# Kernel tuning notes

Measured on AMD Instinct MI355X. Metric: run time of the kernel, lower is better.

Reference implementation:

```python
import jax, jax.numpy as jnp
import numpy as np

B, S, D, E, K = 4, 2048, 1024, 8, 2


def setup_inputs() -> dict:
    key = jax.random.key(0)
    k1, k2, k3 = jax.random.split(key, 3)
    scale = 1.0 / np.sqrt(D)
    x = jax.random.normal(k1, (B, S, D), dtype=jnp.float32)
    Wg = jax.random.normal(k2, (D, E), dtype=jnp.float32) * scale
    bg = jnp.zeros((E,), dtype=jnp.float32)
    We = jax.random.normal(k3, (E, D, D), dtype=jnp.float32) * scale
    be = jnp.zeros((E, D), dtype=jnp.float32)
    return {"x": x, "Wg": Wg, "bg": bg, "We": We, "be": be}


def reference(x, Wg, bg, We, be):
    # gate scores: [B, S, E]
    gate_scores = jnp.einsum("bsd,de->bse", x, Wg) + bg
    topk_values, topk_indices = jax.lax.top_k(gate_scores, K)
    # mask: -inf everywhere except at top-k indices (where value == score)
    sel = jax.nn.one_hot(topk_indices, E, dtype=jnp.bool_).any(axis=-2)  # [B,S,E]
    masked = jnp.where(sel, gate_scores, -jnp.inf)
    gate_weights = jax.nn.softmax(masked, axis=-1)  # [B,S,E]
    # dense all-expert compute, as in the original: [B,S,E,D]
    expert_outputs = jnp.einsum("bsd,edh->bseh", x, We) + be
    fused = jnp.einsum("bse,bseh->bsh", gate_weights, expert_outputs)
    return fused
```

## Files before the change

kernel.cpp:

```cpp
#include <hip/hip_runtime.h>
#include <stdint.h>

#define NTOK   8192
#define DIM    1024
#define NEXP   8
#define MAXP   8192

#define BM 128
#define BN 128
#define BK 32

typedef float  f32x4  __attribute__((ext_vector_type(4)));
typedef __bf16 bf16x8 __attribute__((ext_vector_type(8)));

typedef __attribute__((address_space(1))) const void* gas_ptr;
typedef __attribute__((address_space(3))) void*       las_ptr;

__device__ __forceinline__ unsigned short f32_to_bf16(float f) {
  union { float f; unsigned int u; } v; v.f = f;
  unsigned int u = v.u;
  unsigned int r = (u + 0x7FFFu + ((u >> 16) & 1u)) >> 16;
  return (unsigned short)r;
}

__global__ __launch_bounds__(256) void prep_kernel(
    const float* __restrict__ We, unsigned short* __restrict__ Wt,
    const float* __restrict__ x, const float* __restrict__ Wg,
    const float* __restrict__ bg, unsigned short* __restrict__ Xbf,
    int* __restrict__ tok_ee, float2* __restrict__ tok_w) {
  __shared__ float tile[64][65];
  const int bid = blockIdx.x;
  if (bid < 2048) {
    const int e  = bid >> 8;
    const int d0 = ((bid >> 4) & 15) * 64;
    const int h0 = (bid & 15) * 64;
    const int t  = threadIdx.x;
    const int tx = t & 63, ty = t >> 6;
    const float* src = We + (size_t)e * DIM * DIM;
#pragma unroll
    for (int i = 0; i < 16; ++i) {
      int d = ty + i * 4;
      tile[d][tx] = src[(size_t)(d0 + d) * DIM + (h0 + tx)];
    }
    __syncthreads();
    unsigned short* dst = Wt + (size_t)e * DIM * DIM;
    const int tx2 = t & 31, ty8 = t >> 5;
#pragma unroll
    for (int i = 0; i < 8; ++i) {
      int h = ty8 + i * 8;
      int d = tx2 * 2;
      unsigned int pk = (unsigned int)f32_to_bf16(tile[d][h]) |
                        ((unsigned int)f32_to_bf16(tile[d + 1][h]) << 16);
      *(unsigned int*)&dst[(size_t)(h0 + h) * DIM + d0 + d] = pk;
    }
    return;
  }
  const int blk  = bid - 2048;
  const int wave = threadIdx.x >> 6;
  const int lane = threadIdx.x & 63;
  const int tok  = blk * 4 + wave;

  const float* xr = x + (size_t)tok * DIM + lane * 16;
  float xs[16];
#pragma unroll
  for (int i = 0; i < 4; ++i) *(f32x4*)&xs[i * 4] = *(const f32x4*)(xr + i * 4);

  unsigned int packed[8];
#pragma unroll
  for (int i = 0; i < 8; ++i)
    packed[i] = (unsigned int)f32_to_bf16(xs[2 * i]) |
                ((unsigned int)f32_to_bf16(xs[2 * i + 1]) << 16);
  uint4* xb = (uint4*)(Xbf + (size_t)tok * DIM + lane * 16);
  xb[0] = make_uint4(packed[0], packed[1], packed[2], packed[3]);
  xb[1] = make_uint4(packed[4], packed[5], packed[6], packed[7]);

  double acc[8] = {0, 0, 0, 0, 0, 0, 0, 0};
  const float* wr = Wg + (size_t)(lane * 16) * NEXP;
#pragma unroll
  for (int i = 0; i < 16; ++i) {
    f32x4 wa = *(const f32x4*)(wr + i * 8);
    f32x4 wb = *(const f32x4*)(wr + i * 8 + 4);
    double xd = (double)xs[i];
    acc[0] += xd * (double)wa[0]; acc[1] += xd * (double)wa[1];
    acc[2] += xd * (double)wa[2]; acc[3] += xd * (double)wa[3];
    acc[4] += xd * (double)wb[0]; acc[5] += xd * (double)wb[1];
    acc[6] += xd * (double)wb[2]; acc[7] += xd * (double)wb[3];
  }
#pragma unroll
  for (int m = 1; m < 64; m <<= 1) {
#pragma unroll
    for (int e = 0; e < 8; ++e) acc[e] += __shfl_xor(acc[e], m, 64);
  }

  if (lane == 0) {
    float s[8];
#pragma unroll
    for (int e = 0; e < 8; ++e) s[e] = (float)acc[e] + bg[e];
    int i0 = 0; float v0 = s[0];
#pragma unroll
    for (int e = 1; e < 8; ++e) if (s[e] > v0) { v0 = s[e]; i0 = e; }
    int i1 = -1; float v1 = -3.4e38f;
#pragma unroll
    for (int e = 0; e < 8; ++e) if (e != i0 && s[e] > v1) { v1 = s[e]; i1 = e; }
    float t1 = expf(v1 - v0);
    float den = 1.0f + t1;
    tok_ee[tok] = i0 | (i1 << 8);
    tok_w[tok]  = make_float2(1.0f / den, t1 / den);
  }
}

__global__ __launch_bounds__(1024) void compact_kernel(
    const int* __restrict__ tok_ee, const float2* __restrict__ tok_w,
    int* __restrict__ counts, int* __restrict__ pair_token,
    float* __restrict__ pair_w) {
  __shared__ int wave_cnt[16][NEXP];
  __shared__ int wave_off[16][NEXP];
  __shared__ int base[NEXP];
  __shared__ int chunk_tot[NEXP];
  const int tid = threadIdx.x, wave = tid >> 6, lane = tid & 63;
  if (tid < NEXP) base[tid] = 0;
  __syncthreads();
  for (int c = 0; c < NTOK / 1024; ++c) {
    const int t = c * 1024 + tid;
    const int p = tok_ee[t];
    const int e0 = p & 255, e1 = (p >> 8) & 255;
    const float2 w = tok_w[t];
    int pre0 = 0, pre1 = 0;
    const unsigned long long below = (1ull << lane) - 1ull;
#pragma unroll
    for (int e = 0; e < NEXP; ++e) {
      unsigned long long m = __ballot(e0 == e || e1 == e);
      if (e0 == e) pre0 = __popcll(m & below);
      if (e1 == e) pre1 = __popcll(m & below);
      if (lane == 0) wave_cnt[wave][e] = __popcll(m);
    }
    __syncthreads();
    if (tid < NEXP) {
      int s = 0;
      for (int w2 = 0; w2 < 16; ++w2) {
        wave_off[w2][tid] = s;
        s += wave_cnt[w2][tid];
      }
      chunk_tot[tid] = s;
    }
    __syncthreads();
    const int s0 = base[e0] + wave_off[wave][e0] + pre0;
    const int s1 = base[e1] + wave_off[wave][e1] + pre1;
    pair_token[e0 * MAXP + s0] = (t << 1);     pair_w[e0 * MAXP + s0] = w.x;
    pair_token[e1 * MAXP + s1] = (t << 1) | 1; pair_w[e1 * MAXP + s1] = w.y;
    __syncthreads();
    if (tid < NEXP) base[tid] += chunk_tot[tid];
    __syncthreads();
  }
  if (tid < NEXP) counts[tid] = base[tid];
}

__global__ __launch_bounds__(256) void moe_gemm(
    const unsigned short* __restrict__ Xbf, const unsigned short* __restrict__ Wt,
    const float* __restrict__ be, const int* __restrict__ counts,
    const int* __restrict__ pair_token, const float* __restrict__ pair_w,
    float* __restrict__ part, float* __restrict__ Y, int use_part) {
  const int id  = blockIdx.x;
  const int e   = id & 7;
  const int n0  = ((id >> 3) & 7) * BN;
  const int m0  = (id >> 6) * BM;
  const int cnt = counts[e];
  if (m0 >= cnt) return;

  __shared__ __align__(16) unsigned short As[2][BM * BK];
  __shared__ __align__(16) unsigned short Bs[2][BN * BK];

  const int tid  = threadIdx.x;
  const int wave = tid >> 6;
  const int lane = tid & 63;
  const int fm   = lane & 15;
  const int fq   = lane >> 4;
  const int wm   = wave >> 1;
  const int wn   = wave & 1;

  const int srow = wave * 32 + (lane >> 2);
  const int kc   = (lane & 3) * 8;
  const unsigned short* gA[2];
  const unsigned short* gB[2];
#pragma unroll
  for (int c = 0; c < 2; ++c) {
    int r  = srow + c * 16;
    int gr = m0 + r;
    int tk = (gr < cnt) ? (pair_token[e * MAXP + gr] >> 1) : 0;
    gA[c] = Xbf + (size_t)tk * DIM + kc;
    gB[c] = Wt + (size_t)e * DIM * DIM + (size_t)(n0 + r) * DIM + kc;
  }

#define STAGE(buf, koff)                                                      \
  {                                                                           \
    _Pragma("unroll") for (int c = 0; c < 2; ++c) {                           \
      __builtin_amdgcn_global_load_lds(                                       \
          (gas_ptr)(uintptr_t)(gA[c] + (koff)),                               \
          (las_ptr)(uintptr_t)(&As[buf][(wave * 2 + c) * 512]), 16, 0, 0);    \
      __builtin_amdgcn_global_load_lds(                                       \
          (gas_ptr)(uintptr_t)(gB[c] + (koff)),                               \
          (las_ptr)(uintptr_t)(&Bs[buf][(wave * 2 + c) * 512]), 16, 0, 0);    \
    }                                                                         \
  }

  f32x4 acc[4][4];
#pragma unroll
  for (int i = 0; i < 4; ++i)
#pragma unroll
    for (int j = 0; j < 4; ++j) { f32x4 z = {0.f, 0.f, 0.f, 0.f}; acc[i][j] = z; }

  STAGE(0, 0);
  int cur = 0;
  for (int k0 = 0; k0 < DIM; k0 += BK) {
    __syncthreads();
    if (k0 + BK < DIM) STAGE(cur ^ 1, k0 + BK);

    bf16x8 af[4], bfr[4];
#pragma unroll
    for (int i = 0; i < 4; ++i)
      af[i] = *(const bf16x8*)&As[cur][(wm * 64 + i * 16 + fm) * BK + fq * 8];
#pragma unroll
    for (int j = 0; j < 4; ++j)
      bfr[j] = *(const bf16x8*)&Bs[cur][(wn * 64 + j * 16 + fm) * BK + fq * 8];
#pragma unroll
    for (int i = 0; i < 4; ++i)
#pragma unroll
      for (int j = 0; j < 4; ++j)
        acc[i][j] = __builtin_amdgcn_mfma_f32_16x16x32_bf16(af[i], bfr[j],
                                                            acc[i][j], 0, 0, 0);
    cur ^= 1;
  }
#undef STAGE

  int   rowv[4][4];
  float wrow[4][4];
#pragma unroll
  for (int i = 0; i < 4; ++i)
#pragma unroll
    for (int r = 0; r < 4; ++r) {
      int gr = m0 + wm * 64 + i * 16 + fq * 4 + r;
      bool valid = gr < cnt;
      rowv[i][r] = valid ? pair_token[e * MAXP + gr] : -1;
      wrow[i][r] = valid ? pair_w[e * MAXP + gr] : 0.f;
    }
  if (use_part) {
#pragma unroll
    for (int j = 0; j < 4; ++j) {
      int col = n0 + wn * 64 + j * 16 + fm;
      float bev = be[e * DIM + col];
#pragma unroll
      for (int i = 0; i < 4; ++i)
#pragma unroll
        for (int r = 0; r < 4; ++r) {
          int v = rowv[i][r];
          if (v >= 0)
            part[(size_t)v * DIM + col] = wrow[i][r] * (acc[i][j][r] + bev);
        }
    }
  } else {
#pragma unroll
    for (int j = 0; j < 4; ++j) {
      int col = n0 + wn * 64 + j * 16 + fm;
      float bev = be[e * DIM + col];
#pragma unroll
      for (int i = 0; i < 4; ++i)
#pragma unroll
        for (int r = 0; r < 4; ++r) {
          int v = rowv[i][r];
          if (v >= 0)
            atomicAdd(Y + (size_t)(v >> 1) * DIM + col,
                      wrow[i][r] * (acc[i][j][r] + bev));
        }
    }
  }
}

__global__ __launch_bounds__(256) void reduce_pairs(
    const float* __restrict__ part, float* __restrict__ Y) {
  const int g = blockIdx.x * 256 + threadIdx.x;
  const int t = g >> 8;
  const int o = (g & 255) * 4;
  const f32x4 a = *(const f32x4*)(part + (size_t)(2 * t) * DIM + o);
  const f32x4 b = *(const f32x4*)(part + (size_t)(2 * t + 1) * DIM + o);
  *(f32x4*)(Y + (size_t)t * DIM + o) = a + b;
}

extern "C" void kernel_launch(void* const* d_in, const int* in_sizes, int n_in,
                              void* d_out, int out_size, void* d_ws, size_t ws_size,
                              hipStream_t stream) {
  const float* x  = (const float*)d_in[0];
  const float* Wg = (const float*)d_in[1];
  const float* bg = (const float*)d_in[2];
  const float* We = (const float*)d_in[3];
  const float* be = (const float*)d_in[4];
  float* Y = (float*)d_out;

  const size_t MB = 1024 * 1024;
  char* ws = (char*)d_ws;
  unsigned short* Xbf = (unsigned short*)ws;
  unsigned short* Wt  = (unsigned short*)(ws + 16 * MB);
  const size_t part_bytes = (size_t)NTOK * 2 * DIM * 4;
  const size_t need = 32 * MB + part_bytes + 1 * MB;
  const int use_part = ws_size >= need;
  float* part = (float*)(ws + 32 * MB);
  char* p2 = ws + 32 * MB + (use_part ? part_bytes : 0);
  int*    counts     = (int*)p2;
  int*    pair_token = (int*)(p2 + 256);
  float*  pair_w     = (float*)(p2 + 256 + 262144);
  int*    tok_ee     = (int*)(p2 + 256 + 2 * 262144);
  float2* tok_w      = (float2*)(p2 + 256 + 2 * 262144 + 32768);

  if (!use_part)
    hipMemsetAsync(d_out, 0, (size_t)out_size * sizeof(float), stream);

  prep_kernel<<<4096, 256, 0, stream>>>(We, Wt, x, Wg, bg, Xbf, tok_ee, tok_w);
  compact_kernel<<<1, 1024, 0, stream>>>(tok_ee, tok_w, counts, pair_token,
                                         pair_w);
  moe_gemm<<<dim3(8 * 8 * (NTOK / BM)), 256, 0, stream>>>(
      Xbf, Wt, be, counts, pair_token, pair_w, part, Y, use_part);
  if (use_part)
    reduce_pairs<<<NTOK * DIM / 4 / 256, 256, 0, stream>>>(part, Y);
}
```

Before: 241.5 us.

## Pre-swizzle expert weights into MFMA fragment order and load B directly to registers

The weight-prep pass now writes bf16 expert weights in a layout that matches the MFMA B-fragment order, so each lane's 8-element fragment is contiguous. The GEMM drops the B shared-memory tile and loads B fragments straight from global memory into registers, double-buffered alongside the A staging, with the k-loop unrolled by two. This removes LDS traffic and capacity for B, but each wave now pulls B independently from global memory (the two wm waves duplicate the same loads), relying on cache for reuse.

```diff
diff --git a/kernel.cpp b/kernel.cpp
--- a/kernel.cpp
+++ b/kernel.cpp
@@ -24,7 +24,7 @@
 }
 
 __global__ __launch_bounds__(256) void prep_kernel(
-    const float* __restrict__ We, unsigned short* __restrict__ Wt,
+    const float* __restrict__ We, unsigned short* __restrict__ Wf,
     const float* __restrict__ x, const float* __restrict__ Wg,
     const float* __restrict__ bg, unsigned short* __restrict__ Xbf,
     int* __restrict__ tok_ee, float2* __restrict__ tok_w) {
@@ -43,15 +43,19 @@
       tile[d][tx] = src[(size_t)(d0 + d) * DIM + (h0 + tx)];
     }
     __syncthreads();
-    unsigned short* dst = Wt + (size_t)e * DIM * DIM;
+    unsigned short* dst = Wf + (size_t)e * DIM * DIM;
     const int tx2 = t & 31, ty8 = t >> 5;
 #pragma unroll
     for (int i = 0; i < 8; ++i) {
-      int h = ty8 + i * 8;
-      int d = tx2 * 2;
+      int h  = ty8 + i * 8;
+      int d  = tx2 * 2;
+      int hg = h0 + h, dg = d0 + d;
+      int nj = hg >> 4, fmm = hg & 15;
+      int s  = dg >> 5, fq = (dg >> 3) & 3, el = dg & 7;
+      size_t idx = ((((size_t)nj * 32 + s) * 64 + fq * 16 + fmm) << 3) + el;
       unsigned int pk = (unsigned int)f32_to_bf16(tile[d][h]) |
                         ((unsigned int)f32_to_bf16(tile[d + 1][h]) << 16);
-      *(unsigned int*)&dst[(size_t)(h0 + h) * DIM + d0 + d] = pk;
+      *(unsigned int*)&dst[idx] = pk;
     }
     return;
   }
@@ -156,7 +160,7 @@
 }
 
 __global__ __launch_bounds__(256) void moe_gemm(
-    const unsigned short* __restrict__ Xbf, const unsigned short* __restrict__ Wt,
+    const unsigned short* __restrict__ Xbf, const unsigned short* __restrict__ Wf,
     const float* __restrict__ be, const int* __restrict__ counts,
     const int* __restrict__ pair_token, const float* __restrict__ pair_w,
     float* __restrict__ part, float* __restrict__ Y, int use_part) {
@@ -168,7 +172,6 @@
   if (m0 >= cnt) return;
 
   __shared__ __align__(16) unsigned short As[2][BM * BK];
-  __shared__ __align__(16) unsigned short Bs[2][BN * BK];
 
   const int tid  = threadIdx.x;
   const int wave = tid >> 6;
@@ -178,59 +181,72 @@
   const int wm   = wave >> 1;
   const int wn   = wave & 1;
 
-  const int srow = wave * 32 + (lane >> 2);
-  const int kc   = (lane & 3) * 8;
+  const int kc = (lane & 3) * 8;
   const unsigned short* gA[2];
-  const unsigned short* gB[2];
 #pragma unroll
   for (int c = 0; c < 2; ++c) {
-    int r  = srow + c * 16;
+    int r  = wave * 32 + c * 16 + (lane >> 2);
     int gr = m0 + r;
     int tk = (gr < cnt) ? (pair_token[e * MAXP + gr] >> 1) : 0;
     gA[c] = Xbf + (size_t)tk * DIM + kc;
-    gB[c] = Wt + (size_t)e * DIM * DIM + (size_t)(n0 + r) * DIM + kc;
-  }
-
-#define STAGE(buf, koff)                                                      \
+  }
+
+  const unsigned short* pB[4];
+  const size_t ebase = (size_t)e * DIM * DIM;
+#pragma unroll
+  for (int j = 0; j < 4; ++j) {
+    int njg = (n0 >> 4) + wn * 4 + j;
+    pB[j] = Wf + ebase + (((size_t)njg * 32) * 64 + lane) * 8;
+  }
+
+#define STAGE_A(buf, koff)                                                    \
   {                                                                           \
     _Pragma("unroll") for (int c = 0; c < 2; ++c) {                           \
       __builtin_amdgcn_global_load_lds(                                       \
           (gas_ptr)(uintptr_t)(gA[c] + (koff)),                               \
           (las_ptr)(uintptr_t)(&As[buf][(wave * 2 + c) * 512]), 16, 0, 0);    \
-      __builtin_amdgcn_global_load_lds(                                       \
-          (gas_ptr)(uintptr_t)(gB[c] + (koff)),                               \
-          (las_ptr)(uintptr_t)(&Bs[buf][(wave * 2 + c) * 512]), 16, 0, 0);    \
     }                                                                         \
   }
 
+#define COMPUTE(buf, bq)                                                      \
+  {                                                                           \
+    bf16x8 af[4];                                                             \
+    _Pragma("unroll") for (int i = 0; i < 4; ++i)                             \
+        af[i] = *(const bf16x8*)&As[buf][(wm * 64 + i * 16 + fm) * BK + fq * 8]; \
+    _Pragma("unroll") for (int i = 0; i < 4; ++i)                             \
+      _Pragma("unroll") for (int j = 0; j < 4; ++j)                           \
+        acc[i][j] = __builtin_amdgcn_mfma_f32_16x16x32_bf16(af[i], bq[j],     \
+                                                            acc[i][j], 0, 0, 0); \
+  }
+
   f32x4 acc[4][4];
 #pragma unroll
   for (int i = 0; i < 4; ++i)
 #pragma unroll
     for (int j = 0; j < 4; ++j) { f32x4 z = {0.f, 0.f, 0.f, 0.f}; acc[i][j] = z; }
 
-  STAGE(0, 0);
-  int cur = 0;
-  for (int k0 = 0; k0 < DIM; k0 += BK) {
-    __syncthreads();
-    if (k0 + BK < DIM) STAGE(cur ^ 1, k0 + BK);
-
-    bf16x8 af[4], bfr[4];
-#pragma unroll
-    for (int i = 0; i < 4; ++i)
-      af[i] = *(const bf16x8*)&As[cur][(wm * 64 + i * 16 + fm) * BK + fq * 8];
-#pragma unroll
-    for (int j = 0; j < 4; ++j)
-      bfr[j] = *(const bf16x8*)&Bs[cur][(wn * 64 + j * 16 + fm) * BK + fq * 8];
-#pragma unroll
-    for (int i = 0; i < 4; ++i)
+  bf16x8 b0[4], b1[4];
+#pragma unroll
+  for (int j = 0; j < 4; ++j) b0[j] = *(const bf16x8*)(pB[j]);
+  STAGE_A(0, 0);
+
+  for (int s = 0; s < DIM / BK; s += 2) {
+    __syncthreads();
+    STAGE_A(1, (s + 1) * BK);
+#pragma unroll
+    for (int j = 0; j < 4; ++j) b1[j] = *(const bf16x8*)(pB[j] + (s + 1) * 512);
+    COMPUTE(0, b0);
+    __syncthreads();
+    if (s + 2 < DIM / BK) {
+      STAGE_A(0, (s + 2) * BK);
 #pragma unroll
       for (int j = 0; j < 4; ++j)
-        acc[i][j] = __builtin_amdgcn_mfma_f32_16x16x32_bf16(af[i], bfr[j],
-                                                            acc[i][j], 0, 0, 0);
-    cur ^= 1;
-  }
-#undef STAGE
+        b0[j] = *(const bf16x8*)(pB[j] + (s + 2) * 512);
+    }
+    COMPUTE(1, b1);
+  }
+#undef STAGE_A
+#undef COMPUTE
 
   int   rowv[4][4];
   float wrow[4][4];
@@ -298,7 +314,7 @@
   const size_t MB = 1024 * 1024;
   char* ws = (char*)d_ws;
   unsigned short* Xbf = (unsigned short*)ws;
-  unsigned short* Wt  = (unsigned short*)(ws + 16 * MB);
+  unsigned short* Wf  = (unsigned short*)(ws + 16 * MB);
   const size_t part_bytes = (size_t)NTOK * 2 * DIM * 4;
   const size_t need = 32 * MB + part_bytes + 1 * MB;
   const int use_part = ws_size >= need;
@@ -313,11 +329,11 @@
   if (!use_part)
     hipMemsetAsync(d_out, 0, (size_t)out_size * sizeof(float), stream);
 
-  prep_kernel<<<4096, 256, 0, stream>>>(We, Wt, x, Wg, bg, Xbf, tok_ee, tok_w);
+  prep_kernel<<<4096, 256, 0, stream>>>(We, Wf, x, Wg, bg, Xbf, tok_ee, tok_w);
   compact_kernel<<<1, 1024, 0, stream>>>(tok_ee, tok_w, counts, pair_token,
                                          pair_w);
   moe_gemm<<<dim3(8 * 8 * (NTOK / BM)), 256, 0, stream>>>(
-      Xbf, Wt, be, counts, pair_token, pair_w, part, Y, use_part);
+      Xbf, Wf, be, counts, pair_token, pair_w, part, Y, use_part);
   if (use_part)
     reduce_pairs<<<NTOK * DIM / 4 / 256, 256, 0, stream>>>(part, Y);
 }
```

New measurement: 249.0 us. +3.1%, slower.

## Pre-swizzle operands into MFMA fragment layout and drop LDS staging in GEMM

Applied to the files above, without the earlier changes.

The weight-prep pass now writes expert weights in bf16 directly in MFMA fragment order. A new regather kernel packs each expert's routed token rows into fragment-ordered tiles, with per-expert tile offsets recorded in counts. The GEMM then loads fragments straight from global memory into registers with one-step register double buffering, replacing LDS staging and barriers. This removes LDS traffic and synchronisation, but adds an extra kernel, about 32 MB of workspace, and duplicated global/L2 loads across waves that no longer share tiles through LDS. reduce_pairs is also changed to process four elements per thread over a smaller grid.

```diff
diff --git a/kernel.cpp b/kernel.cpp
--- a/kernel.cpp
+++ b/kernel.cpp
@@ -8,13 +8,9 @@
 
 #define BM 128
 #define BN 128
-#define BK 32
 
 typedef float  f32x4  __attribute__((ext_vector_type(4)));
 typedef __bf16 bf16x8 __attribute__((ext_vector_type(8)));
-
-typedef __attribute__((address_space(1))) const void* gas_ptr;
-typedef __attribute__((address_space(3))) void*       las_ptr;
 
 __device__ __forceinline__ unsigned short f32_to_bf16(float f) {
   union { float f; unsigned int u; } v; v.f = f;
@@ -24,7 +20,7 @@
 }
 
 __global__ __launch_bounds__(256) void prep_kernel(
-    const float* __restrict__ We, unsigned short* __restrict__ Wt,
+    const float* __restrict__ We, unsigned short* __restrict__ Wf,
     const float* __restrict__ x, const float* __restrict__ Wg,
     const float* __restrict__ bg, unsigned short* __restrict__ Xbf,
     int* __restrict__ tok_ee, float2* __restrict__ tok_w) {
@@ -43,15 +39,23 @@
       tile[d][tx] = src[(size_t)(d0 + d) * DIM + (h0 + tx)];
     }
     __syncthreads();
-    unsigned short* dst = Wt + (size_t)e * DIM * DIM;
-    const int tx2 = t & 31, ty8 = t >> 5;
-#pragma unroll
-    for (int i = 0; i < 8; ++i) {
-      int h = ty8 + i * 8;
-      int d = tx2 * 2;
-      unsigned int pk = (unsigned int)f32_to_bf16(tile[d][h]) |
-                        ((unsigned int)f32_to_bf16(tile[d + 1][h]) << 16);
-      *(unsigned int*)&dst[(size_t)(h0 + h) * DIM + d0 + d] = pk;
+    const int w = t >> 6, lane = t & 63;
+    const int fm = lane & 15, fq = lane >> 4;
+#pragma unroll
+    for (int p = 0; p < 2; ++p) {
+      int idxl = w * 2 + p;
+      int njl = idxl >> 1, sl = idxl & 1;
+      int hl  = njl * 16 + fm;
+      unsigned int pk[4];
+#pragma unroll
+      for (int q = 0; q < 4; ++q) {
+        int dl = sl * 32 + fq * 8 + q * 2;
+        pk[q] = (unsigned int)f32_to_bf16(tile[dl][hl]) |
+                ((unsigned int)f32_to_bf16(tile[dl + 1][hl]) << 16);
+      }
+      int nj = (h0 >> 4) + njl, s = (d0 >> 5) + sl;
+      size_t idx = (((size_t)nj * 32 + s) * 64 + lane) * 8;
+      *(uint4*)&Wf[((size_t)e << 20) + idx] = make_uint4(pk[0], pk[1], pk[2], pk[3]);
     }
     return;
   }
@@ -153,10 +157,45 @@
     __syncthreads();
   }
   if (tid < NEXP) counts[tid] = base[tid];
+  __syncthreads();
+  if (tid == 0) {
+    int run = 0;
+    for (int e = 0; e < NEXP; ++e) { counts[8 + e] = run; run += (base[e] + 127) >> 7; }
+  }
+}
+
+__global__ __launch_bounds__(256) void regather(
+    const unsigned short* __restrict__ Xbf, const int* __restrict__ counts,
+    const int* __restrict__ pair_token, unsigned short* __restrict__ Af) {
+  const int id   = blockIdx.x;
+  const int e    = id & 7;
+  const int half = (id >> 3) & 1;
+  const int mt   = id >> 4;
+  const int cnt  = counts[e];
+  const int m0   = mt * BM;
+  if (m0 >= cnt) return;
+  const int tile = counts[8 + e] + mt;
+
+  const int wave = threadIdx.x >> 6;
+  const int lane = threadIdx.x & 63;
+  const int fm   = lane & 15, fq = lane >> 4;
+  const int ri   = half * 4 + wave;
+
+  const int gr = m0 + ri * 16 + fm;
+  const int pt = (gr < cnt) ? (pair_token[e * MAXP + gr] >> 1) : -1;
+  const unsigned short* src = Xbf + (size_t)(pt < 0 ? 0 : pt) * DIM + fq * 8;
+  unsigned short* dst = Af + (size_t)tile * 131072 + ((size_t)ri * 32) * 512 + lane * 8;
+
+#pragma unroll 4
+  for (int s = 0; s < 32; ++s) {
+    uint4 v = make_uint4(0, 0, 0, 0);
+    if (pt >= 0) v = *(const uint4*)(src + s * 32);
+    *(uint4*)(dst + s * 512) = v;
+  }
 }
 
 __global__ __launch_bounds__(256) void moe_gemm(
-    const unsigned short* __restrict__ Xbf, const unsigned short* __restrict__ Wt,
+    const unsigned short* __restrict__ Af, const unsigned short* __restrict__ Wf,
     const float* __restrict__ be, const int* __restrict__ counts,
     const int* __restrict__ pair_token, const float* __restrict__ pair_w,
     float* __restrict__ part, float* __restrict__ Y, int use_part) {
@@ -166,9 +205,7 @@
   const int m0  = (id >> 6) * BM;
   const int cnt = counts[e];
   if (m0 >= cnt) return;
-
-  __shared__ __align__(16) unsigned short As[2][BM * BK];
-  __shared__ __align__(16) unsigned short Bs[2][BN * BK];
+  const int tile = counts[8 + e] + (m0 >> 7);
 
   const int tid  = threadIdx.x;
   const int wave = tid >> 6;
@@ -178,30 +215,10 @@
   const int wm   = wave >> 1;
   const int wn   = wave & 1;
 
-  const int srow = wave * 32 + (lane >> 2);
-  const int kc   = (lane & 3) * 8;
-  const unsigned short* gA[2];
-  const unsigned short* gB[2];
-#pragma unroll
-  for (int c = 0; c < 2; ++c) {
-    int r  = srow + c * 16;
-    int gr = m0 + r;
-    int tk = (gr < cnt) ? (pair_token[e * MAXP + gr] >> 1) : 0;
-    gA[c] = Xbf + (size_t)tk * DIM + kc;
-    gB[c] = Wt + (size_t)e * DIM * DIM + (size_t)(n0 + r) * DIM + kc;
-  }
-
-#define STAGE(buf, koff)                                                      \
-  {                                                                           \
-    _Pragma("unroll") for (int c = 0; c < 2; ++c) {                           \
-      __builtin_amdgcn_global_load_lds(                                       \
-          (gas_ptr)(uintptr_t)(gA[c] + (koff)),                               \
-          (las_ptr)(uintptr_t)(&As[buf][(wave * 2 + c) * 512]), 16, 0, 0);    \
-      __builtin_amdgcn_global_load_lds(                                       \
-          (gas_ptr)(uintptr_t)(gB[c] + (koff)),                               \
-          (las_ptr)(uintptr_t)(&Bs[buf][(wave * 2 + c) * 512]), 16, 0, 0);    \
-    }                                                                         \
-  }
+  const unsigned short* baseA = Af + (size_t)tile * 131072 + lane * 8;
+  const unsigned short* baseB = Wf + ((size_t)e << 20) + lane * 8;
+  const int ri0 = wm * 4;
+  const int nj0 = (n0 >> 4) + wn * 4;
 
   f32x4 acc[4][4];
 #pragma unroll
@@ -209,28 +226,32 @@
 #pragma unroll
     for (int j = 0; j < 4; ++j) { f32x4 z = {0.f, 0.f, 0.f, 0.f}; acc[i][j] = z; }
 
-  STAGE(0, 0);
-  int cur = 0;
-  for (int k0 = 0; k0 < DIM; k0 += BK) {
-    __syncthreads();
-    if (k0 + BK < DIM) STAGE(cur ^ 1, k0 + BK);
-
-    bf16x8 af[4], bfr[4];
+  bf16x8 a[2][4], b[2][4];
+#pragma unroll
+  for (int i = 0; i < 4; ++i)
+    a[0][i] = *(const bf16x8*)(baseA + (size_t)((ri0 + i) * 32) * 512);
+#pragma unroll
+  for (int j = 0; j < 4; ++j)
+    b[0][j] = *(const bf16x8*)(baseB + (size_t)((nj0 + j) * 32) * 512);
+
+#pragma unroll
+  for (int s = 0; s < 32; ++s) {
+    const int cur = s & 1, nxt = cur ^ 1;
+    if (s + 1 < 32) {
+#pragma unroll
+      for (int i = 0; i < 4; ++i)
+        a[nxt][i] = *(const bf16x8*)(baseA + (size_t)((ri0 + i) * 32 + s + 1) * 512);
+#pragma unroll
+      for (int j = 0; j < 4; ++j)
+        b[nxt][j] = *(const bf16x8*)(baseB + (size_t)((nj0 + j) * 32 + s + 1) * 512);
+    }
 #pragma unroll
     for (int i = 0; i < 4; ++i)
-      af[i] = *(const bf16x8*)&As[cur][(wm * 64 + i * 16 + fm) * BK + fq * 8];
-#pragma unroll
-    for (int j = 0; j < 4; ++j)
-      bfr[j] = *(const bf16x8*)&Bs[cur][(wn * 64 + j * 16 + fm) * BK + fq * 8];
-#pragma unroll
-    for (int i = 0; i < 4; ++i)
 #pragma unroll
       for (int j = 0; j < 4; ++j)
-        acc[i][j] = __builtin_amdgcn_mfma_f32_16x16x32_bf16(af[i], bfr[j],
+        acc[i][j] = __builtin_amdgcn_mfma_f32_16x16x32_bf16(a[cur][i], b[cur][j],
                                                             acc[i][j], 0, 0, 0);
-    cur ^= 1;
-  }
-#undef STAGE
+  }
 
   int   rowv[4][4];
   float wrow[4][4];
@@ -277,12 +298,16 @@
 
 __global__ __launch_bounds__(256) void reduce_pairs(
     const float* __restrict__ part, float* __restrict__ Y) {
-  const int g = blockIdx.x * 256 + threadIdx.x;
-  const int t = g >> 8;
-  const int o = (g & 255) * 4;
-  const f32x4 a = *(const f32x4*)(part + (size_t)(2 * t) * DIM + o);
-  const f32x4 b = *(const f32x4*)(part + (size_t)(2 * t + 1) * DIM + o);
-  *(f32x4*)(Y + (size_t)t * DIM + o) = a + b;
+  const int g0 = blockIdx.x * 256 + threadIdx.x;
+#pragma unroll
+  for (int it = 0; it < 4; ++it) {
+    const int g = g0 + it * (2048 * 256);
+    const int t = g >> 8;
+    const int o = (g & 255) * 4;
+    const f32x4 a = *(const f32x4*)(part + (size_t)(2 * t) * DIM + o);
+    const f32x4 b = *(const f32x4*)(part + (size_t)(2 * t + 1) * DIM + o);
+    *(f32x4*)(Y + (size_t)t * DIM + o) = a + b;
+  }
 }
 
 extern "C" void kernel_launch(void* const* d_in, const int* in_sizes, int n_in,
@@ -298,12 +323,13 @@
   const size_t MB = 1024 * 1024;
   char* ws = (char*)d_ws;
   unsigned short* Xbf = (unsigned short*)ws;
-  unsigned short* Wt  = (unsigned short*)(ws + 16 * MB);
+  unsigned short* Wf  = (unsigned short*)(ws + 16 * MB);
+  unsigned short* Af  = (unsigned short*)(ws + 32 * MB);
   const size_t part_bytes = (size_t)NTOK * 2 * DIM * 4;
-  const size_t need = 32 * MB + part_bytes + 1 * MB;
-  const int use_part = ws_size >= need;
-  float* part = (float*)(ws + 32 * MB);
-  char* p2 = ws + 32 * MB + (use_part ? part_bytes : 0);
+  const size_t need_full = 68 * MB + part_bytes + 1 * MB;
+  const int use_part = ws_size >= need_full;
+  float* part = (float*)(ws + 68 * MB);
+  char* p2 = ws + 68 * MB + (use_part ? part_bytes : 0);
   int*    counts     = (int*)p2;
   int*    pair_token = (int*)(p2 + 256);
   float*  pair_w     = (float*)(p2 + 256 + 262144);
@@ -313,11 +339,12 @@
   if (!use_part)
     hipMemsetAsync(d_out, 0, (size_t)out_size * sizeof(float), stream);
 
-  prep_kernel<<<4096, 256, 0, stream>>>(We, Wt, x, Wg, bg, Xbf, tok_ee, tok_w);
+  prep_kernel<<<4096, 256, 0, stream>>>(We, Wf, x, Wg, bg, Xbf, tok_ee, tok_w);
   compact_kernel<<<1, 1024, 0, stream>>>(tok_ee, tok_w, counts, pair_token,
                                          pair_w);
-  moe_gemm<<<dim3(8 * 8 * (NTOK / BM)), 256, 0, stream>>>(
-      Xbf, Wt, be, counts, pair_token, pair_w, part, Y, use_part);
+  regather<<<NEXP * 2 * (MAXP / BM), 256, 0, stream>>>(Xbf, counts, pair_token, Af);
+  moe_gemm<<<8 * 8 * (NTOK / BM), 256, 0, stream>>>(
+      Af, Wf, be, counts, pair_token, pair_w, part, Y, use_part);
   if (use_part)
-    reduce_pairs<<<NTOK * DIM / 4 / 256, 256, 0, stream>>>(part, Y);
-}
+    reduce_pairs<<<2048, 256, 0, stream>>>(part, Y);
+}
```

Result: slower. 317.1 us (+31.3%).
